# Performance work log

Measured on AMD Instinct MI355X. Metric: run time of the kernel, lower is better.

The kernel has to match this reference:

```python
import jax, jax.numpy as jnp
import numpy as np

N = 49152
F = 128            # num_features (multiplicity of every irrep)
DIMS = (1, 3, 5)   # 2l+1 for l = 0, 1, 2
L = len(DIMS)
D = sum(DIMS)      # 9 components per channel

# tp1 per-component scale: w3j(l,l,0) = 1/sqrt(2l+1), e3nn path norm over 3 paths -> 1/sqrt(3)
_C1 = np.concatenate([np.full(d, (2 * l + 1) ** -0.5, np.float32) for l, d in enumerate(DIMS)]) / np.float32(np.sqrt(3.0))
_INV_SQRT_F = np.float32(F ** -0.5)  # e3nn o3.Linear fan-in normalization


def _irrep_linear(x, W):
    # x: [N, F, D], W: [L, F, F] (one channel-mixing matrix per degree, block-diagonal over degrees)
    outs, o = [], 0
    for l, d in enumerate(DIMS):
        outs.append(jnp.einsum('nud,vu->nvd', x[:, :, o:o + d], W[l]) * _INV_SQRT_F)
        o += d
    return jnp.concatenate(outs, axis=-1)


def setup_inputs() -> dict:
    key = jax.random.key(0)
    ks = jax.random.split(key, 10)
    xav = np.float32((2.0 / (F + 2 * F)) ** 0.5)   # xavier_uniform-ish scale for ls
    xav2 = np.float32((2.0 / (F + F)) ** 0.5)      # for lvs
    return {
        'T':     jax.random.normal(ks[0], (N, F, D), jnp.float32),
        'S':     jax.random.normal(ks[1], (N, F), jnp.float32),
        'Wq':    jax.random.normal(ks[2], (L, F, F), jnp.float32),
        'Wk':    jax.random.normal(ks[3], (L, F, F), jnp.float32),
        'Wv':    jax.random.normal(ks[4], (L, F, F), jnp.float32),
        'w2':    jax.random.normal(ks[5], (L, F), jnp.float32),   # tp2 'uuu' path weights
        'ls_w':  jax.random.normal(ks[6], (2 * F, F), jnp.float32) * xav,
        'ls_b':  jnp.zeros((2 * F,), jnp.float32),
        'lvs_w': jax.random.normal(ks[7], (F, F), jnp.float32) * xav2,
        'lvs_b': jnp.zeros((F,), jnp.float32),
    }


def reference(T, S, Wq, Wk, Wv, w2, ls_w, ls_b, lvs_w, lvs_b):
    q = _irrep_linear(T, Wq)                 # [N, F, D]
    k = _irrep_linear(T, Wk)
    v = _irrep_linear(T, Wv)
    # tp1: per-channel inner product over m, summed over degrees with per-degree w3j scale
    s = jnp.einsum('nud,nud,d->nu', q, k, jnp.asarray(_C1))   # [N, F]
    p = jax.nn.softmax(s @ ls_w.T + ls_b, axis=-1)            # [N, 2F]
    su, sd = p[:, :F], p[:, F:]
    # tp2: scalar (per-channel) gate times irrep values, learnable per-(degree,channel) weight
    w2c = jnp.concatenate([jnp.repeat(w2[l][:, None], d, axis=1) for l, d in enumerate(DIMS)], axis=1)  # [F, D]
    tu = sd[:, :, None] * v * w2c[None]                       # [N, F, D]
    out2 = su * jax.nn.silu(S @ lvs_w.T + lvs_b)              # [N, F]
    return tu, out2
```

## Files before the change

### kernel.cpp

```cpp
#include <hip/hip_runtime.h>

#define N_NODES 49152
#define FDIM    128
#define DDIM    9
#define NB      16
#define NBLK    (N_NODES / NB)
#define OUT2_OFF ((size_t)N_NODES * FDIM * DDIM)

#define WQ_OFF   0
#define WK_OFF   49152
#define WV_OFF   98304
#define LS_OFF   147456
#define LVS_OFF  180224
#define WS_ELEMS 196608

typedef __bf16 bf16x8 __attribute__((ext_vector_type(8)));
typedef float  floatx4 __attribute__((ext_vector_type(4)));

__device__ __forceinline__ unsigned short f2bf(float f) {
    unsigned u = __float_as_uint(f);
    u += 0x7FFFu + ((u >> 16) & 1u);
    return (unsigned short)(u >> 16);
}

__device__ __forceinline__ floatx4 mfma16(bf16x8 a, bf16x8 b, floatx4 c) {
    return __builtin_amdgcn_mfma_f32_16x16x32_bf16(a, b, c, 0, 0, 0);
}

__global__ void prep_kernel(const float* __restrict__ Wq, const float* __restrict__ Wk,
                            const float* __restrict__ Wv, const float* __restrict__ lsw,
                            const float* __restrict__ lvw, unsigned short* __restrict__ ws) {
    int i = blockIdx.x * 256 + threadIdx.x;
    if (i >= WS_ELEMS) return;
    float v;
    if      (i < WK_OFF)  v = Wq[i - WQ_OFF];
    else if (i < WV_OFF)  v = Wk[i - WK_OFF];
    else if (i < LS_OFF)  v = Wv[i - WV_OFF];
    else if (i < LVS_OFF) v = lsw[i - LS_OFF];
    else                  v = lvw[i - LVS_OFF];
    ws[i] = f2bf(v);
}

struct SMem {
    union {
        unsigned short ttr[NB * DDIM * 136];
        float tu8[8 * 1160];
    } u;
    unsigned short sS[NB * 136];
    unsigned short sbuf[NB * 136];
    float p[NB * 273];
    float w2l[3 * FDIM];
    float redA[4 * 16];
    float redB[4 * 16];
};

__global__ void __launch_bounds__(256, 2)
tpattn_main(const float* __restrict__ T, const float* __restrict__ S,
            const float* __restrict__ w2, const float* __restrict__ ls_b,
            const float* __restrict__ lvs_b, const unsigned short* __restrict__ wbf,
            float* __restrict__ out) {
    __shared__ SMem sm;
    const int tid  = threadIdx.x;
    const int w    = tid >> 6;
    const int lane = tid & 63;
    const int quad = lane >> 4;
    const int m16  = lane & 15;
    const int n0   = blockIdx.x * NB;

    const unsigned short* Wq  = wbf + WQ_OFF;
    const unsigned short* Wk  = wbf + WK_OFF;
    const unsigned short* Wv  = wbf + WV_OFF;
    const unsigned short* Lsw = wbf + LS_OFF;
    const unsigned short* Lvw = wbf + LVS_OFF;

    constexpr int   DL[3]  = {1, 3, 5};
    constexpr int   OL[3]  = {0, 1, 4};
    constexpr float C1A[3] = {0.57735026919f, 0.33333333333f, 0.25819888975f};
    const float INV_F  = 0.0078125f;
    const float INV_SF = 0.08838834764831845f;

    {
        const float4* Tg = (const float4*)(T + (size_t)n0 * 1152);
        #pragma unroll
        for (int it = 0; it < 18; ++it) {
            int lin = (it * 256 + tid) * 4;
            float4 val = Tg[it * 256 + tid];
            float vv[4] = {val.x, val.y, val.z, val.w};
            #pragma unroll
            for (int e = 0; e < 4; ++e) {
                int le = lin + e;
                int t9 = le / 9;
                int dd = le - t9 * 9;
                int n  = t9 >> 7;
                int uu = t9 & 127;
                sm.u.ttr[(n * 9 + dd) * 136 + uu] = f2bf(vv[e]);
            }
        }
        const float4* Sg = (const float4*)(S + (size_t)n0 * 128);
        #pragma unroll
        for (int it = 0; it < 2; ++it) {
            int lin = (it * 256 + tid) * 4;
            float4 val = Sg[it * 256 + tid];
            int n = lin >> 7, uu = lin & 127;
            sm.sS[n * 136 + uu + 0] = f2bf(val.x);
            sm.sS[n * 136 + uu + 1] = f2bf(val.y);
            sm.sS[n * 136 + uu + 2] = f2bf(val.z);
            sm.sS[n * 136 + uu + 3] = f2bf(val.w);
        }
        for (int i = tid; i < 3 * FDIM; i += 256) sm.w2l[i] = w2[i];
    }
    __syncthreads();

    float sf[2][4] = {{0.f,0.f,0.f,0.f},{0.f,0.f,0.f,0.f}};
    #pragma unroll
    for (int l = 0; l < 3; ++l) {
        bf16x8 aq[2][4], ak[2][4];
        #pragma unroll
        for (int vt = 0; vt < 2; ++vt)
            #pragma unroll
            for (int kc = 0; kc < 4; ++kc) {
                int v  = w * 32 + vt * 16 + m16;
                int u0 = kc * 32 + quad * 8;
                aq[vt][kc] = *(const bf16x8*)(Wq + (l * 128 + v) * 128 + u0);
                ak[vt][kc] = *(const bf16x8*)(Wk + (l * 128 + v) * 128 + u0);
            }
        #pragma unroll
        for (int j = 0; j < DL[l]; ++j) {
            int jj = OL[l] + j;
            bf16x8 b[4];
            #pragma unroll
            for (int kc = 0; kc < 4; ++kc)
                b[kc] = *(const bf16x8*)(&sm.u.ttr[(m16 * 9 + jj) * 136 + kc * 32 + quad * 8]);
            floatx4 q0 = {0.f,0.f,0.f,0.f}, q1 = {0.f,0.f,0.f,0.f};
            floatx4 k0 = {0.f,0.f,0.f,0.f}, k1 = {0.f,0.f,0.f,0.f};
            #pragma unroll
            for (int kc = 0; kc < 4; ++kc) {
                q0 = mfma16(aq[0][kc], b[kc], q0);
                q1 = mfma16(aq[1][kc], b[kc], q1);
                k0 = mfma16(ak[0][kc], b[kc], k0);
                k1 = mfma16(ak[1][kc], b[kc], k1);
            }
            #pragma unroll
            for (int r = 0; r < 4; ++r) {
                sf[0][r] += C1A[l] * q0[r] * k0[r];
                sf[1][r] += C1A[l] * q1[r] * k1[r];
            }
        }
    }
    #pragma unroll
    for (int vt = 0; vt < 2; ++vt)
        #pragma unroll
        for (int r = 0; r < 4; ++r) {
            int uu = w * 32 + vt * 16 + quad * 4 + r;
            sm.sbuf[m16 * 136 + uu] = f2bf(sf[vt][r] * INV_F);
        }
    __syncthreads();

    float lg[4][4];
    {
        bf16x8 bs[4];
        #pragma unroll
        for (int kc = 0; kc < 4; ++kc)
            bs[kc] = *(const bf16x8*)(&sm.sbuf[m16 * 136 + kc * 32 + quad * 8]);
        #pragma unroll
        for (int rt = 0; rt < 4; ++rt) {
            floatx4 acc = {0.f,0.f,0.f,0.f};
            int ia = (4 * w + rt) * 16 + m16;
            #pragma unroll
            for (int kc = 0; kc < 4; ++kc) {
                bf16x8 a = *(const bf16x8*)(Lsw + ia * 128 + kc * 32 + quad * 8);
                acc = mfma16(a, bs[kc], acc);
            }
            int i0 = (4 * w + rt) * 16 + quad * 4;
            float4 bias = *(const float4*)(ls_b + i0);
            lg[rt][0] = acc[0] + bias.x;
            lg[rt][1] = acc[1] + bias.y;
            lg[rt][2] = acc[2] + bias.z;
            lg[rt][3] = acc[3] + bias.w;
        }
    }

    {
        float mx = lg[0][0];
        #pragma unroll
        for (int rt = 0; rt < 4; ++rt)
            #pragma unroll
            for (int r = 0; r < 4; ++r) mx = fmaxf(mx, lg[rt][r]);
        mx = fmaxf(mx, __shfl_xor(mx, 16, 64));
        mx = fmaxf(mx, __shfl_xor(mx, 32, 64));
        if (lane < 16) sm.redA[w * 16 + lane] = mx;
        __syncthreads();
        float m4 = fmaxf(fmaxf(sm.redA[m16], sm.redA[16 + m16]),
                         fmaxf(sm.redA[32 + m16], sm.redA[48 + m16]));
        float lsum = 0.f;
        #pragma unroll
        for (int rt = 0; rt < 4; ++rt)
            #pragma unroll
            for (int r = 0; r < 4; ++r) {
                float e = __expf(lg[rt][r] - m4);
                lg[rt][r] = e;
                lsum += e;
            }
        lsum += __shfl_xor(lsum, 16, 64);
        lsum += __shfl_xor(lsum, 32, 64);
        if (lane < 16) sm.redB[w * 16 + lane] = lsum;
        __syncthreads();
        float tot = sm.redB[m16] + sm.redB[16 + m16] + sm.redB[32 + m16] + sm.redB[48 + m16];
        float rinv = 1.0f / tot;
        #pragma unroll
        for (int rt = 0; rt < 4; ++rt)
            #pragma unroll
            for (int r = 0; r < 4; ++r)
                sm.p[m16 * 273 + (4 * w + rt) * 16 + quad * 4 + r] = lg[rt][r] * rinv;
    }
    __syncthreads();

    float sdv[2][4];
    float w2v[3][2][4];
    #pragma unroll
    for (int vt = 0; vt < 2; ++vt)
        #pragma unroll
        for (int r = 0; r < 4; ++r) {
            int uu = w * 32 + vt * 16 + quad * 4 + r;
            sdv[vt][r] = sm.p[m16 * 273 + 128 + uu] * INV_SF;
            #pragma unroll
            for (int l = 0; l < 3; ++l) w2v[l][vt][r] = sm.w2l[l * 128 + uu];
        }

    floatx4 vacc[9][2];
    #pragma unroll
    for (int l = 0; l < 3; ++l) {
        bf16x8 av[2][4];
        #pragma unroll
        for (int vt = 0; vt < 2; ++vt)
            #pragma unroll
            for (int kc = 0; kc < 4; ++kc) {
                int v  = w * 32 + vt * 16 + m16;
                int u0 = kc * 32 + quad * 8;
                av[vt][kc] = *(const bf16x8*)(Wv + (l * 128 + v) * 128 + u0);
            }
        #pragma unroll
        for (int j = 0; j < DL[l]; ++j) {
            int jj = OL[l] + j;
            bf16x8 b[4];
            #pragma unroll
            for (int kc = 0; kc < 4; ++kc)
                b[kc] = *(const bf16x8*)(&sm.u.ttr[(m16 * 9 + jj) * 136 + kc * 32 + quad * 8]);
            floatx4 a0 = {0.f,0.f,0.f,0.f}, a1 = {0.f,0.f,0.f,0.f};
            #pragma unroll
            for (int kc = 0; kc < 4; ++kc) {
                a0 = mfma16(av[0][kc], b[kc], a0);
                a1 = mfma16(av[1][kc], b[kc], a1);
            }
            vacc[jj][0] = a0;
            vacc[jj][1] = a1;
        }
    }
    __syncthreads();

    #pragma unroll
    for (int h = 0; h < 2; ++h) {
        if (((m16 >> 3) & 1) == h) {
            int n8 = m16 & 7;
            #pragma unroll
            for (int l = 0; l < 3; ++l)
                #pragma unroll
                for (int j = 0; j < DL[l]; ++j) {
                    int jj = OL[l] + j;
                    #pragma unroll
                    for (int vt = 0; vt < 2; ++vt)
                        #pragma unroll
                        for (int r = 0; r < 4; ++r) {
                            int uu = w * 32 + vt * 16 + quad * 4 + r;
                            sm.u.tu8[n8 * 1160 + uu * 9 + jj] =
                                vacc[jj][vt][r] * sdv[vt][r] * w2v[l][vt][r];
                        }
                }
        }
        __syncthreads();
        float* outt = out + (size_t)(n0 + h * 8) * 1152;
        #pragma unroll
        for (int it = 0; it < 9; ++it) {
            int lin = it * 1024 + tid * 4;
            int n8  = lin / 1152;
            int r   = lin - n8 * 1152;
            float4 v4 = *(const float4*)(&sm.u.tu8[n8 * 1160 + r]);
            *(float4*)(outt + (size_t)n8 * 1152 + r) = v4;
        }
        __syncthreads();
    }

    {
        bf16x8 bS[4];
        #pragma unroll
        for (int kc = 0; kc < 4; ++kc)
            bS[kc] = *(const bf16x8*)(&sm.sS[m16 * 136 + kc * 32 + quad * 8]);
        #pragma unroll
        for (int rt = 0; rt < 2; ++rt) {
            floatx4 acc = {0.f,0.f,0.f,0.f};
            int ia = (2 * w + rt) * 16 + m16;
            #pragma unroll
            for (int kc = 0; kc < 4; ++kc) {
                bf16x8 a = *(const bf16x8*)(Lvw + ia * 128 + kc * 32 + quad * 8);
                acc = mfma16(a, bS[kc], acc);
            }
            int i0 = (2 * w + rt) * 16 + quad * 4;
            float4 bias = *(const float4*)(lvs_b + i0);
            float bb[4] = {bias.x, bias.y, bias.z, bias.w};
            float o4[4];
            #pragma unroll
            for (int r = 0; r < 4; ++r) {
                float z   = acc[r] + bb[r];
                float sig = 1.0f / (1.0f + __expf(-z));
                float su  = sm.p[m16 * 273 + i0 + r];
                o4[r] = su * z * sig;
            }
            *(float4*)(out + OUT2_OFF + (size_t)(n0 + m16) * 128 + i0) =
                make_float4(o4[0], o4[1], o4[2], o4[3]);
        }
    }
}

extern "C" void kernel_launch(void* const* d_in, const int* in_sizes, int n_in,
                              void* d_out, int out_size, void* d_ws, size_t ws_size,
                              hipStream_t stream) {
    const float* T   = (const float*)d_in[0];
    const float* S   = (const float*)d_in[1];
    const float* Wq  = (const float*)d_in[2];
    const float* Wk  = (const float*)d_in[3];
    const float* Wv  = (const float*)d_in[4];
    const float* w2  = (const float*)d_in[5];
    const float* lsw = (const float*)d_in[6];
    const float* lsb = (const float*)d_in[7];
    const float* lvw = (const float*)d_in[8];
    const float* lvb = (const float*)d_in[9];
    float* out = (float*)d_out;
    unsigned short* wbf = (unsigned short*)d_ws;

    if (ws_size < WS_ELEMS * sizeof(unsigned short)) return;

    prep_kernel<<<(WS_ELEMS + 255) / 256, 256, 0, stream>>>(Wq, Wk, Wv, lsw, lvw, wbf);
    tpattn_main<<<NBLK, 256, 0, stream>>>(T, S, w2, lsb, lvb, wbf, out);
}
```

Baseline: 564.8 us.

## Keep softmax probs in registers and write tu directly from MFMA accumulators

```diff
diff --git a/kernel.cpp b/kernel.cpp
--- a/kernel.cpp
+++ b/kernel.cpp
@@ -16,6 +16,7 @@
 
 typedef __bf16 bf16x8 __attribute__((ext_vector_type(8)));
 typedef float  floatx4 __attribute__((ext_vector_type(4)));
+typedef unsigned short ushortx4 __attribute__((ext_vector_type(4)));
 
 __device__ __forceinline__ unsigned short f2bf(float f) {
     unsigned u = __float_as_uint(f);
@@ -42,19 +43,15 @@
 }
 
 struct SMem {
-    union {
-        unsigned short ttr[NB * DDIM * 136];
-        float tu8[8 * 1160];
-    } u;
+    unsigned short ttr[NB * DDIM * 136];
     unsigned short sS[NB * 136];
     unsigned short sbuf[NB * 136];
-    float p[NB * 273];
     float w2l[3 * FDIM];
-    float redA[4 * 16];
-    float redB[4 * 16];
+    float redA[64];
+    float redB[64];
 };
 
-__global__ void __launch_bounds__(256, 2)
+__global__ void __launch_bounds__(256, 3)
 tpattn_main(const float* __restrict__ T, const float* __restrict__ S,
             const float* __restrict__ w2, const float* __restrict__ ls_b,
             const float* __restrict__ lvs_b, const unsigned short* __restrict__ wbf,
@@ -81,20 +78,21 @@
 
     {
         const float4* Tg = (const float4*)(T + (size_t)n0 * 1152);
+        int t9 = (tid * 4) / 9;
+        int dd = tid * 4 - t9 * 9;
         #pragma unroll
         for (int it = 0; it < 18; ++it) {
-            int lin = (it * 256 + tid) * 4;
             float4 val = Tg[it * 256 + tid];
             float vv[4] = {val.x, val.y, val.z, val.w};
+            int t9c = t9, ddc = dd;
             #pragma unroll
             for (int e = 0; e < 4; ++e) {
-                int le = lin + e;
-                int t9 = le / 9;
-                int dd = le - t9 * 9;
-                int n  = t9 >> 7;
-                int uu = t9 & 127;
-                sm.u.ttr[(n * 9 + dd) * 136 + uu] = f2bf(vv[e]);
-            }
+                int n  = t9c >> 7;
+                int uu = t9c & 127;
+                sm.ttr[(n * 9 + ddc) * 136 + uu] = f2bf(vv[e]);
+                ++ddc; if (ddc == 9) { ddc = 0; ++t9c; }
+            }
+            t9 += 113; dd += 7; if (dd >= 9) { dd -= 9; ++t9; }
         }
         const float4* Sg = (const float4*)(S + (size_t)n0 * 128);
         #pragma unroll
@@ -102,10 +100,8 @@
             int lin = (it * 256 + tid) * 4;
             float4 val = Sg[it * 256 + tid];
             int n = lin >> 7, uu = lin & 127;
-            sm.sS[n * 136 + uu + 0] = f2bf(val.x);
-            sm.sS[n * 136 + uu + 1] = f2bf(val.y);
-            sm.sS[n * 136 + uu + 2] = f2bf(val.z);
-            sm.sS[n * 136 + uu + 3] = f2bf(val.w);
+            ushortx4 pk = { f2bf(val.x), f2bf(val.y), f2bf(val.z), f2bf(val.w) };
+            *(ushortx4*)(&sm.sS[n * 136 + uu]) = pk;
         }
         for (int i = tid; i < 3 * FDIM; i += 256) sm.w2l[i] = w2[i];
     }
@@ -130,7 +126,7 @@
             bf16x8 b[4];
             #pragma unroll
             for (int kc = 0; kc < 4; ++kc)
-                b[kc] = *(const bf16x8*)(&sm.u.ttr[(m16 * 9 + jj) * 136 + kc * 32 + quad * 8]);
+                b[kc] = *(const bf16x8*)(&sm.ttr[(m16 * 9 + jj) * 136 + kc * 32 + quad * 8]);
             floatx4 q0 = {0.f,0.f,0.f,0.f}, q1 = {0.f,0.f,0.f,0.f};
             floatx4 k0 = {0.f,0.f,0.f,0.f}, k1 = {0.f,0.f,0.f,0.f};
             #pragma unroll
@@ -164,14 +160,15 @@
             bs[kc] = *(const bf16x8*)(&sm.sbuf[m16 * 136 + kc * 32 + quad * 8]);
         #pragma unroll
         for (int rt = 0; rt < 4; ++rt) {
+            int tile = (rt < 2) ? (2 * w + rt) : (6 + 2 * w + rt);
             floatx4 acc = {0.f,0.f,0.f,0.f};
-            int ia = (4 * w + rt) * 16 + m16;
+            int ia = tile * 16 + m16;
             #pragma unroll
             for (int kc = 0; kc < 4; ++kc) {
                 bf16x8 a = *(const bf16x8*)(Lsw + ia * 128 + kc * 32 + quad * 8);
                 acc = mfma16(a, bs[kc], acc);
             }
-            int i0 = (4 * w + rt) * 16 + quad * 4;
+            int i0 = tile * 16 + quad * 4;
             float4 bias = *(const float4*)(ls_b + i0);
             lg[rt][0] = acc[0] + bias.x;
             lg[rt][1] = acc[1] + bias.y;
@@ -211,21 +208,15 @@
         for (int rt = 0; rt < 4; ++rt)
             #pragma unroll
             for (int r = 0; r < 4; ++r)
-                sm.p[m16 * 273 + (4 * w + rt) * 16 + quad * 4 + r] = lg[rt][r] * rinv;
-    }
-    __syncthreads();
+                lg[rt][r] *= rinv;
+    }
 
     float sdv[2][4];
-    float w2v[3][2][4];
     #pragma unroll
     for (int vt = 0; vt < 2; ++vt)
         #pragma unroll
-        for (int r = 0; r < 4; ++r) {
-            int uu = w * 32 + vt * 16 + quad * 4 + r;
-            sdv[vt][r] = sm.p[m16 * 273 + 128 + uu] * INV_SF;
-            #pragma unroll
-            for (int l = 0; l < 3; ++l) w2v[l][vt][r] = sm.w2l[l * 128 + uu];
-        }
+        for (int r = 0; r < 4; ++r)
+            sdv[vt][r] = lg[2 + vt][r] * INV_SF;
 
     floatx4 vacc[9][2];
     #pragma unroll
@@ -245,7 +236,7 @@
             bf16x8 b[4];
             #pragma unroll
             for (int kc = 0; kc < 4; ++kc)
-                b[kc] = *(const bf16x8*)(&sm.u.ttr[(m16 * 9 + jj) * 136 + kc * 32 + quad * 8]);
+                b[kc] = *(const bf16x8*)(&sm.ttr[(m16 * 9 + jj) * 136 + kc * 32 + quad * 8]);
             floatx4 a0 = {0.f,0.f,0.f,0.f}, a1 = {0.f,0.f,0.f,0.f};
             #pragma unroll
             for (int kc = 0; kc < 4; ++kc) {
@@ -256,38 +247,31 @@
             vacc[jj][1] = a1;
         }
     }
-    __syncthreads();
-
-    #pragma unroll
-    for (int h = 0; h < 2; ++h) {
-        if (((m16 >> 3) & 1) == h) {
-            int n8 = m16 & 7;
-            #pragma unroll
-            for (int l = 0; l < 3; ++l)
+
+    {
+        float* outn = out + (size_t)(n0 + m16) * 1152;
+        #pragma unroll
+        for (int vt = 0; vt < 2; ++vt) {
+            int u0 = w * 32 + vt * 16 + quad * 4;
+            float vals[36];
+            #pragma unroll
+            for (int r = 0; r < 4; ++r) {
+                int uu = u0 + r;
+                float c0 = sdv[vt][r] * sm.w2l[uu];
+                float c1 = sdv[vt][r] * sm.w2l[128 + uu];
+                float c2 = sdv[vt][r] * sm.w2l[256 + uu];
+                vals[r * 9 + 0] = vacc[0][vt][r] * c0;
                 #pragma unroll
-                for (int j = 0; j < DL[l]; ++j) {
-                    int jj = OL[l] + j;
-                    #pragma unroll
-                    for (int vt = 0; vt < 2; ++vt)
-                        #pragma unroll
-                        for (int r = 0; r < 4; ++r) {
-                            int uu = w * 32 + vt * 16 + quad * 4 + r;
-                            sm.u.tu8[n8 * 1160 + uu * 9 + jj] =
-                                vacc[jj][vt][r] * sdv[vt][r] * w2v[l][vt][r];
-                        }
-                }
-        }
-        __syncthreads();
-        float* outt = out + (size_t)(n0 + h * 8) * 1152;
-        #pragma unroll
-        for (int it = 0; it < 9; ++it) {
-            int lin = it * 1024 + tid * 4;
-            int n8  = lin / 1152;
-            int r   = lin - n8 * 1152;
-            float4 v4 = *(const float4*)(&sm.u.tu8[n8 * 1160 + r]);
-            *(float4*)(outt + (size_t)n8 * 1152 + r) = v4;
-        }
-        __syncthreads();
+                for (int j = 0; j < 3; ++j) vals[r * 9 + 1 + j] = vacc[1 + j][vt][r] * c1;
+                #pragma unroll
+                for (int j = 0; j < 5; ++j) vals[r * 9 + 4 + j] = vacc[4 + j][vt][r] * c2;
+            }
+            float4* dst = (float4*)(outn + (size_t)u0 * 9);
+            #pragma unroll
+            for (int q4 = 0; q4 < 9; ++q4)
+                dst[q4] = make_float4(vals[q4 * 4 + 0], vals[q4 * 4 + 1],
+                                      vals[q4 * 4 + 2], vals[q4 * 4 + 3]);
+        }
     }
 
     {
@@ -312,7 +296,7 @@
             for (int r = 0; r < 4; ++r) {
                 float z   = acc[r] + bb[r];
                 float sig = 1.0f / (1.0f + __expf(-z));
-                float su  = sm.p[m16 * 273 + i0 + r];
+                float su  = lg[rt][r];
                 o4[r] = su * z * sig;
             }
             *(float4*)(out + OUT2_OFF + (size_t)(n0 + m16) * 128 + i0) =
```

Result: slower. 595.1 us (+5.4%).
